# Kernel tuning notes

Measured on AMD Instinct MI355X. Metric: run time of the kernel, lower is better.

The kernel has to match this reference:

```python
import jax, jax.numpy as jnp
import numpy as np

B, S, H = 1, 4096, 2048
NH, NKV, HD = 16, 4, 128  # query heads, kv heads, head_dim
THETA = 1000000.0
NEG = -1e9


def setup_inputs() -> dict:
    key = jax.random.key(0)
    ks = jax.random.split(key, 5)
    hidden_states = jax.random.normal(ks[0], (B, S, H), jnp.float32) * 0.02
    Wq = jax.random.normal(ks[1], (H, NH * HD), jnp.float32) * 0.02
    Wk = jax.random.normal(ks[2], (H, NKV * HD), jnp.float32) * 0.02
    Wv = jax.random.normal(ks[3], (H, NKV * HD), jnp.float32) * 0.02
    Wo = jax.random.normal(ks[4], (H, H), jnp.float32) * 0.02
    # additive causal mask [B,1,S,S]
    causal = jnp.tril(jnp.ones((S, S), bool))
    attention_mask = jnp.where(causal, 0.0, NEG).astype(jnp.float32)[None, None]
    position_ids = jnp.arange(S, dtype=jnp.int32)[None]
    return dict(hidden_states=hidden_states, Wq=Wq, Wk=Wk, Wv=Wv, Wo=Wo,
                attention_mask=attention_mask, position_ids=position_ids)


def _rotate_half(x):
    return jnp.concatenate([-x[..., HD // 2:], x[..., :HD // 2]], axis=-1)


def reference(hidden_states, Wq, Wk, Wv, Wo, attention_mask, position_ids):
    # projections -> [B, heads, S, HD]
    q = (hidden_states @ Wq).reshape(B, S, NH, HD).transpose(0, 2, 1, 3)
    k = (hidden_states @ Wk).reshape(B, S, NKV, HD).transpose(0, 2, 1, 3)
    v = (hidden_states @ Wv).reshape(B, S, NKV, HD).transpose(0, 2, 1, 3)

    # RoPE (HF style: freqs duplicated across halves, rotate_half)
    inv_freq = 1.0 / (THETA ** (jnp.arange(0, HD, 2, dtype=jnp.float32) / HD))
    freqs = position_ids.astype(jnp.float32)[..., None] * inv_freq  # [B,S,HD/2]
    emb = jnp.concatenate([freqs, freqs], axis=-1)                  # [B,S,HD]
    cos = jnp.cos(emb)[:, None].astype(q.dtype)                     # [B,1,S,HD]
    sin = jnp.sin(emb)[:, None].astype(q.dtype)
    q = q * cos + _rotate_half(q) * sin
    k = k * cos + _rotate_half(k) * sin

    # GQA: repeat each kv head consecutively (matches torch repeat_kv)
    rep = NH // NKV
    k = jnp.repeat(k, rep, axis=1)
    v = jnp.repeat(v, rep, axis=1)

    scale = 1.0 / jnp.sqrt(jnp.float32(HD))
    scores = jnp.einsum('bhqd,bhkd->bhqk', q, k) * scale + attention_mask
    attn = jax.nn.softmax(scores.astype(jnp.float32), axis=-1).astype(q.dtype)
    out = jnp.einsum('bhqk,bhkd->bhqd', attn, v)  # [B,NH,S,HD]
    out = out.transpose(0, 2, 1, 3).reshape(B, S, H)
    return out @ Wo
```

## Files before the change

### kernel.cpp

```cpp
#include <hip/hip_runtime.h>
#include <stdint.h>

typedef uint16_t u16;
typedef __bf16  bf16x8 __attribute__((ext_vector_type(8)));
typedef float   f32x4  __attribute__((ext_vector_type(4)));
typedef float   f32x16 __attribute__((ext_vector_type(16)));
typedef uint16_t u16x8 __attribute__((ext_vector_type(8), may_alias));
typedef uint32_t u32x4 __attribute__((ext_vector_type(4)));

typedef const __attribute__((address_space(1))) void* gas_p;
typedef __attribute__((address_space(3))) void* las_p;

#define SCALE2 0.1275430214486847f

__device__ __forceinline__ void load_lds16(const void* g, void* l) {
    __builtin_amdgcn_global_load_lds((gas_p)g, (las_p)l, 16, 0, 0);
}

__device__ __forceinline__ u16 f2bf(float f) {
    uint32_t u = __builtin_bit_cast(uint32_t, f);
    u += 0x7FFFu + ((u >> 16) & 1u);
    return (u16)(u >> 16);
}
__device__ __forceinline__ float bf2f(u16 h) {
    uint32_t u = ((uint32_t)h) << 16;
    return __builtin_bit_cast(float, u);
}
__device__ __forceinline__ bf16x8 ld_frag(const u16* p) {
    u16x8 t = *(const u16x8*)p;
    return __builtin_bit_cast(bf16x8, t);
}
__device__ __forceinline__ uint32_t cvt_pk_bf16(float lo, float hi) {
    uint32_t r;
    asm("v_cvt_pk_bf16_f32 %0, %1, %2" : "=v"(r) : "v"(lo), "v"(hi));
    return r;
}
__device__ __forceinline__ void plane32_swap(uint32_t& a, uint32_t& b) {
    asm("v_permlane32_swap_b32 %0, %1" : "+v"(a), "+v"(b));
}

__global__ __launch_bounds__(256) void convert_hidden(const float* __restrict__ in,
                                                      u16* __restrict__ out, int n8) {
    int i = blockIdx.x * 256 + threadIdx.x;
    if (i >= n8) return;
    const float* p = in + (size_t)i * 8;
    u16x8 o;
#pragma unroll
    for (int j = 0; j < 8; j++) o[j] = f2bf(p[j]);
    *(u16x8*)(out + (size_t)i * 8) = o;
}

__global__ __launch_bounds__(256) void transpose_cvt(const float* __restrict__ in,
                                                     u16* __restrict__ out,
                                                     int R, int C) {
    __shared__ u16 tile[64][65];
    const int tx = threadIdx.x;
    const int bc = blockIdx.x * 64;
    const int br = blockIdx.y * 64;
#pragma unroll
    for (int i = 0; i < 16; i++) {
        int idx = tx + i * 256;
        int r = idx >> 6, c = idx & 63;
        tile[r][c] = f2bf(in[(size_t)(br + r) * C + bc + c]);
    }
    __syncthreads();
#pragma unroll
    for (int i = 0; i < 16; i++) {
        int idx = tx + i * 256;
        int r = idx >> 6, c = idx & 63;
        out[(size_t)(bc + r) * R + br + c] = tile[c][r];
    }
}

__global__ __launch_bounds__(256) void transpose_b16(const u16* __restrict__ in,
                                                     u16* __restrict__ out,
                                                     int R, int C, int ldin, int off) {
    __shared__ u16 tile[64][65];
    const int tx = threadIdx.x;
    const int bc = blockIdx.x * 64;
    const int br = blockIdx.y * 64;
#pragma unroll
    for (int i = 0; i < 16; i++) {
        int idx = tx + i * 256;
        int r = idx >> 6, c = idx & 63;
        tile[r][c] = in[(size_t)(br + r) * ldin + off + bc + c];
    }
    __syncthreads();
#pragma unroll
    for (int i = 0; i < 16; i++) {
        int idx = tx + i * 256;
        int r = idx >> 6, c = idx & 63;
        out[(size_t)(bc + r) * R + br + c] = tile[c][r];
    }
}

#define TM 128
#define TN 128
#define TK 32

__global__ __launch_bounds__(256) void gemm_qkv(const u16* __restrict__ A,
                                                const u16* __restrict__ WqT,
                                                const u16* __restrict__ WkvT,
                                                u16* __restrict__ Qb,
                                                u16* __restrict__ KVb) {
    __shared__ u16 As[TM * TK];
    __shared__ u16 Bs[TN * TK];
    const int K = 2048;
    const int tid  = threadIdx.x;
    const int wave = tid >> 6;
    const int lane = tid & 63;
    const int l15  = lane & 15;
    const int quad = lane >> 4;
    const int m0 = blockIdx.y * TM;
    const int n0 = blockIdx.x * TN;
    const u16* Bt;
    u16* C;
    int ldC, cbase;
    if (n0 < 2048) { Bt = WqT + (size_t)n0 * K;          C = Qb;  ldC = 2048; cbase = n0; }
    else           { Bt = WkvT + (size_t)(n0 - 2048) * K; C = KVb; ldC = 1024; cbase = n0 - 2048; }
    const int wm = (wave >> 1) * 64;
    const int wn = (wave & 1) * 64;

    f32x4 acc[4][4] = {};

    const int srow = tid >> 2;
    const int scol = (tid & 3) * 8;
    const u16* Ap0 = A  + (size_t)(m0 + srow) * K + scol;
    const u16* Ap1 = A  + (size_t)(m0 + 64 + srow) * K + scol;
    const u16* Bp0 = Bt + (size_t)srow * K + scol;
    const u16* Bp1 = Bt + (size_t)(64 + srow) * K + scol;
    u16* AsD0 = As + wave * 512;
    u16* AsD1 = As + 2048 + wave * 512;
    u16* BsD0 = Bs + wave * 512;
    u16* BsD1 = Bs + 2048 + wave * 512;

    for (int k0 = 0; k0 < K; k0 += TK) {
        load_lds16(Ap0 + k0, AsD0);
        load_lds16(Ap1 + k0, AsD1);
        load_lds16(Bp0 + k0, BsD0);
        load_lds16(Bp1 + k0, BsD1);
        __syncthreads();
        bf16x8 af[4], bfr[4];
#pragma unroll
        for (int i = 0; i < 4; i++)
            af[i] = ld_frag(&As[(wm + i * 16 + l15) * TK + quad * 8]);
#pragma unroll
        for (int j = 0; j < 4; j++)
            bfr[j] = ld_frag(&Bs[(wn + j * 16 + l15) * TK + quad * 8]);
#pragma unroll
        for (int i = 0; i < 4; i++)
#pragma unroll
            for (int j = 0; j < 4; j++)
                acc[i][j] = __builtin_amdgcn_mfma_f32_16x16x32_bf16(af[i], bfr[j], acc[i][j], 0, 0, 0);
        __syncthreads();
    }
#pragma unroll
    for (int i = 0; i < 4; i++)
#pragma unroll
        for (int j = 0; j < 4; j++)
#pragma unroll
            for (int r = 0; r < 4; r++) {
                int row = m0 + wm + i * 16 + quad * 4 + r;
                int col = cbase + wn + j * 16 + l15;
                C[(size_t)row * ldC + col] = f2bf(acc[i][j][r]);
            }
}

template <bool F32OUT>
__global__ __launch_bounds__(256) void gemm_bt(const u16* __restrict__ A,
                                               const u16* __restrict__ Bt,
                                               void* __restrict__ Cp,
                                               int M, int N, int K) {
    __shared__ u16 As[TM * TK];
    __shared__ u16 Bs[TN * TK];
    const int tid  = threadIdx.x;
    const int wave = tid >> 6;
    const int lane = tid & 63;
    const int l15  = lane & 15;
    const int quad = lane >> 4;
    const int m0 = blockIdx.y * TM;
    const int n0 = blockIdx.x * TN;
    const int wm = (wave >> 1) * 64;
    const int wn = (wave & 1) * 64;

    f32x4 acc[4][4] = {};

    const int srow = tid >> 2;
    const int scol = (tid & 3) * 8;
    const u16* Ap0 = A  + (size_t)(m0 + srow) * K + scol;
    const u16* Ap1 = A  + (size_t)(m0 + 64 + srow) * K + scol;
    const u16* Bp0 = Bt + (size_t)(n0 + srow) * K + scol;
    const u16* Bp1 = Bt + (size_t)(n0 + 64 + srow) * K + scol;
    u16* AsD0 = As + wave * 512;
    u16* AsD1 = As + 2048 + wave * 512;
    u16* BsD0 = Bs + wave * 512;
    u16* BsD1 = Bs + 2048 + wave * 512;

    for (int k0 = 0; k0 < K; k0 += TK) {
        load_lds16(Ap0 + k0, AsD0);
        load_lds16(Ap1 + k0, AsD1);
        load_lds16(Bp0 + k0, BsD0);
        load_lds16(Bp1 + k0, BsD1);
        __syncthreads();
        bf16x8 af[4], bfr[4];
#pragma unroll
        for (int i = 0; i < 4; i++)
            af[i] = ld_frag(&As[(wm + i * 16 + l15) * TK + quad * 8]);
#pragma unroll
        for (int j = 0; j < 4; j++)
            bfr[j] = ld_frag(&Bs[(wn + j * 16 + l15) * TK + quad * 8]);
#pragma unroll
        for (int i = 0; i < 4; i++)
#pragma unroll
            for (int j = 0; j < 4; j++)
                acc[i][j] = __builtin_amdgcn_mfma_f32_16x16x32_bf16(af[i], bfr[j], acc[i][j], 0, 0, 0);
        __syncthreads();
    }
#pragma unroll
    for (int i = 0; i < 4; i++)
#pragma unroll
        for (int j = 0; j < 4; j++)
#pragma unroll
            for (int r = 0; r < 4; r++) {
                int row = m0 + wm + i * 16 + quad * 4 + r;
                int col = n0 + wn + j * 16 + l15;
                if (F32OUT)
                    ((float*)Cp)[(size_t)row * N + col] = acc[i][j][r];
                else
                    ((u16*)Cp)[(size_t)row * N + col] = f2bf(acc[i][j][r]);
            }
}

__global__ __launch_bounds__(256) void rope_kernel(u16* __restrict__ Q,
                                                   u16* __restrict__ KV) {
    int g = blockIdx.x * 256 + threadIdx.x;
    int d = g & 63;
    int row = g >> 6;
    int s = row / 20;
    int hh = row - s * 20;
    u16* buf = (hh < 16) ? (Q + (size_t)s * 2048 + hh * 128)
                         : (KV + (size_t)s * 1024 + (hh - 16) * 128);
    float p = (float)s;
    float angle = p * exp2f((float)d * (-19.931568569324174f / 64.0f));
    float sc = (hh < 16) ? SCALE2 : 1.0f;
    float c = cosf(angle) * sc, sn = sinf(angle) * sc;
    float x0 = bf2f(buf[d]), x1 = bf2f(buf[d + 64]);
    buf[d]      = f2bf(x0 * c - x1 * sn);
    buf[d + 64] = f2bf(x1 * c + x0 * sn);
}


#define SMAX(CC, SV, QG, PA, LACC, MSK)                                        \
  do {                                                                         \
    float p_[16]; float rs_ = 0.f;                                             \
    const int qrow_ = (QG) + l31;                                              \
    const int kvbs_ = kv0 + (CC) * 32 + 4 * hi8;                               \
    _Pragma("unroll")                                                          \
    for (int r = 0; r < 16; r++) {                                             \
      float pe = exp2f((SV)[r]);                                               \
      if (MSK) { int kvv = kvbs_ + (r & 3) + 8 * (r >> 2);                     \
                 pe = (kvv <= qrow_) ? pe : 0.f; }                             \
      p_[r] = pe; rs_ += pe;                                                   \
    }                                                                          \
    LACC += rs_;                                                               \
    uint32_t w0 = cvt_pk_bf16(p_[0], p_[1]);                                   \
    uint32_t w1 = cvt_pk_bf16(p_[2], p_[3]);                                   \
    uint32_t w2 = cvt_pk_bf16(p_[4], p_[5]);                                   \
    uint32_t w3 = cvt_pk_bf16(p_[6], p_[7]);                                   \
    plane32_swap(w0, w2); plane32_swap(w1, w3);                                \
    uint32_t w4 = cvt_pk_bf16(p_[8], p_[9]);                                   \
    uint32_t w5 = cvt_pk_bf16(p_[10], p_[11]);                                 \
    uint32_t w6 = cvt_pk_bf16(p_[12], p_[13]);                                 \
    uint32_t w7 = cvt_pk_bf16(p_[14], p_[15]);                                 \
    plane32_swap(w4, w6); plane32_swap(w5, w7);                                \
    u32x4 a0_ = {w0, w1, w2, w3}, a1_ = {w4, w5, w6, w7};                      \
    PA[0] = __builtin_bit_cast(bf16x8, a0_);                                   \
    PA[1] = __builtin_bit_cast(bf16x8, a1_);                                   \
  } while (0)

#define QK_CHUNK(CC, DOA, DOB, MSK)                                            \
  do {                                                                         \
    const int krow_ = (CC) * 32 + l31;                                         \
    f32x16 svA_ = {}, svB_ = {};                                               \
    _Pragma("unroll")                                                          \
    for (int dk = 0; dk < 8; dk++) {                                           \
      bf16x8 kf = ld_frag(&Kb[krow_ * 128 + (((dk * 2 + hi8) + krow_) & 15) * 8]); \
      if (DOA) svA_ = __builtin_amdgcn_mfma_f32_32x32x16_bf16(kf, qfA[dk], svA_, 0, 0, 0); \
      if (DOB) svB_ = __builtin_amdgcn_mfma_f32_32x32x16_bf16(kf, qfB[dk], svB_, 0, 0, 0); \
    }                                                                          \
    bf16x8 paA_[2], paB_[2];                                                   \
    if (DOA) SMAX((CC), svA_, qg0A, paA_, lrA, (MSK));                         \
    if (DOB) SMAX((CC), svB_, qg0B, paB_, lrB, (MSK));                         \
    _Pragma("unroll")                                                          \
    for (int ks2 = 0; ks2 < 2; ks2++) {                                        \
      _Pragma("unroll")                                                        \
      for (int nt = 0; nt < 4; nt++) {                                         \
        const int d_ = nt * 32 + l31;                                          \
        bf16x8 vf = ld_frag(&Vb[d_ * 64 + ((((CC) * 4 + ks2 * 2 + hi8) + d_) & 7) * 8]); \
        if (DOA) accA[nt] = __builtin_amdgcn_mfma_f32_32x32x16_bf16(paA_[ks2], vf, accA[nt], 0, 0, 0); \
        if (DOB) accB[nt] = __builtin_amdgcn_mfma_f32_32x32x16_bf16(paB_[ks2], vf, accB[nt], 0, 0, 0); \
      }                                                                        \
    }                                                                          \
  } while (0)

__global__ __launch_bounds__(256, 1) void flash_attn5(const u16* __restrict__ Q,
                                                      const u16* __restrict__ KVb,
                                                      const u16* __restrict__ VT,
                                                      u16* __restrict__ O) {
    __shared__ u16 Ks[2][8192];
    __shared__ u16 Vs[2][8192];
    __shared__ float Llds[4][2][32];
    const int tid  = threadIdx.x;
    const int wave = tid >> 6;
    const int lane = tid & 63;
    const int l31  = lane & 31;
    const int hi8  = lane >> 5;
    const int bx   = blockIdx.x;
    const int h    = blockIdx.y;
    const int kvh  = h >> 2;
    const int qg0A = bx * 128 + wave * 32;
    const int qg0B = 3968 - bx * 128 + wave * 32;
    const int dA   = qg0A >> 6;
    const int dB   = qg0B >> 6;
    const int nkv  = 64 - 2 * bx;

    bf16x8 qfA[8], qfB[8];
    {
        const u16* pa = Q + (size_t)(qg0A + l31) * 2048 + h * 128 + hi8 * 8;
        const u16* pb = Q + (size_t)(qg0B + l31) * 2048 + h * 128 + hi8 * 8;
#pragma unroll
        for (int dk = 0; dk < 8; dk++) {
            qfA[dk] = ld_frag(pa + dk * 16);
            qfB[dk] = ld_frag(pb + dk * 16);
        }
    }

    const u16* srcK[4];
    const u16* srcV[4];
#pragma unroll
    for (int r = 0; r < 4; r++) {
        int p = r * 256 + tid;
        int kv = p >> 4;
        srcK[r] = KVb + (size_t)kv * 1024 + kvh * 128 + ((((p & 15) - kv) & 15) * 8);
        int d = p >> 3;
        srcV[r] = VT + (size_t)(kvh * 128 + d) * 4096 + ((((p & 7) - (d & 7)) & 7) * 8);
    }

    f32x16 accA[4] = {}, accB[4] = {};
    float lrA = 0.f, lrB = 0.f;

#pragma unroll
    for (int r = 0; r < 4; r++) {
        load_lds16(srcK[r], &Ks[0][r * 2048 + wave * 512]);
        load_lds16(srcV[r], &Vs[0][r * 2048 + wave * 512]);
    }
    asm volatile("s_waitcnt vmcnt(0)" ::: "memory");
    __syncthreads();

    for (int kvb = 0; kvb < nkv; kvb++) {
        const int cur = kvb & 1;
        if (kvb + 1 < nkv) {
            const int kvn = (kvb + 1) * 64;
#pragma unroll
            for (int r = 0; r < 4; r++) {
                load_lds16(srcK[r] + (size_t)kvn * 1024, &Ks[cur ^ 1][r * 2048 + wave * 512]);
                load_lds16(srcV[r] + kvn, &Vs[cur ^ 1][r * 2048 + wave * 512]);
            }
        }
        const u16* Kb = Ks[cur];
        const u16* Vb = Vs[cur];
        const int kv0 = kvb * 64;

        if (kvb == dA || kvb == dB) {
            QK_CHUNK(0, 1, 1, 1);
            QK_CHUNK(1, 1, 1, 1);
        } else if (kvb < dA) {
            QK_CHUNK(0, 1, 1, 0);
            QK_CHUNK(1, 1, 1, 0);
        } else if (kvb < dB) {
            QK_CHUNK(0, 0, 1, 0);
            QK_CHUNK(1, 0, 1, 0);
        }

        asm volatile("s_waitcnt vmcnt(0)" ::: "memory");
        __syncthreads();
    }

    float ltA = lrA + __shfl_xor(lrA, 32);
    float ltB = lrB + __shfl_xor(lrB, 32);
    if (lane < 32) {
        Llds[wave][0][l31] = ltA;
        Llds[wave][1][l31] = ltB;
    }
    __syncthreads();
#pragma unroll
    for (int r = 0; r < 16; r++) {
        int qr = (r & 3) + 8 * (r >> 2) + 4 * hi8;
        float liA = 1.0f / Llds[wave][0][qr];
        float liB = 1.0f / Llds[wave][1][qr];
        u16* opA = O + (size_t)(qg0A + qr) * 2048 + h * 128 + l31;
        u16* opB = O + (size_t)(qg0B + qr) * 2048 + h * 128 + l31;
#pragma unroll
        for (int nt = 0; nt < 4; nt++) {
            opA[nt * 32] = f2bf(accA[nt][r] * liA);
            opB[nt * 32] = f2bf(accB[nt][r] * liB);
        }
    }
}

extern "C" void kernel_launch(void* const* d_in, const int* in_sizes, int n_in,
                              void* d_out, int out_size, void* d_ws, size_t ws_size,
                              hipStream_t stream) {
    const float* hidden = (const float*)d_in[0];
    const float* Wq = (const float*)d_in[1];
    const float* Wk = (const float*)d_in[2];
    const float* Wv = (const float*)d_in[3];
    const float* Wo = (const float*)d_in[4];
    float* out = (float*)d_out;

    u16* ws   = (u16*)d_ws;
    u16* Hb   = ws;
    u16* Qb   = Hb   + 8388608;
    u16* KVb  = Qb   + 8388608;
    u16* WqT  = KVb  + 4194304;
    u16* WkvT = WqT  + 4194304;
    u16* VT   = WkvT + 2097152;

    convert_hidden<<<4096, 256, 0, stream>>>(hidden, Hb, 1048576);

    transpose_cvt<<<dim3(32, 32), 256, 0, stream>>>(Wq, WqT, 2048, 2048);
    transpose_cvt<<<dim3(8, 32), 256, 0, stream>>>(Wk, WkvT, 2048, 512);
    transpose_cvt<<<dim3(8, 32), 256, 0, stream>>>(Wv, WkvT + 1048576, 2048, 512);

    gemm_qkv<<<dim3(24, 32), 256, 0, stream>>>(Hb, WqT, WkvT, Qb, KVb);

    u16* WoT = WqT;
    transpose_cvt<<<dim3(32, 32), 256, 0, stream>>>(Wo, WoT, 2048, 2048);

    rope_kernel<<<dim3(20480), 256, 0, stream>>>(Qb, KVb);

    transpose_b16<<<dim3(8, 64), 256, 0, stream>>>(KVb, VT, 4096, 512, 1024, 512);

    u16* Ob = Hb;
    flash_attn5<<<dim3(16, 16), 256, 0, stream>>>(Qb, KVb, VT, Ob);

    gemm_bt<true><<<dim3(16, 32), 256, 0, stream>>>(Ob, WoT, out, 4096, 2048, 2048);
}
```

Measured before the change: 435.0 us.

## Split KV range across two wave groups per block in flash attention

The attention block grows from 4 to 8 waves. Each group of 4 waves handles alternate 64-key blocks of a 128-key pair loaded per iteration, so the same query tiles are processed with twice the wave-level parallelism. This targets low occupancy and latency exposure, since the grid has only 256 blocks. Partial accumulators and row sums from group 1 are reduced through LDS scratch into group 0 before normalization and store. That adds LDS traffic, a larger LDS footprint and an extra barrier at the end. There is also some load imbalance when one group's block lies past the causal diagonal.

```diff
diff --git a/kernel.cpp b/kernel.cpp
--- a/kernel.cpp
+++ b/kernel.cpp
@@ -271,8 +271,9 @@
     uint32_t w4 = cvt_pk_bf16(p_[8], p_[9]);                                   \
     uint32_t w5 = cvt_pk_bf16(p_[10], p_[11]);                                 \
     uint32_t w6 = cvt_pk_bf16(p_[12], p_[13]);                                 \
+    plane32_swap(w4, w6);                                                      \
     uint32_t w7 = cvt_pk_bf16(p_[14], p_[15]);                                 \
-    plane32_swap(w4, w6); plane32_swap(w5, w7);                                \
+    plane32_swap(w5, w7);                                                      \
     u32x4 a0_ = {w0, w1, w2, w3}, a1_ = {w4, w5, w6, w7};                      \
     PA[0] = __builtin_bit_cast(bf16x8, a0_);                                   \
     PA[1] = __builtin_bit_cast(bf16x8, a1_);                                   \
@@ -296,33 +297,36 @@
       _Pragma("unroll")                                                        \
       for (int nt = 0; nt < 4; nt++) {                                         \
         const int d_ = nt * 32 + l31;                                          \
-        bf16x8 vf = ld_frag(&Vb[d_ * 64 + ((((CC) * 4 + ks2 * 2 + hi8) + d_) & 7) * 8]); \
+        const int vc_ = g * 8 + (CC) * 4 + ks2 * 2 + hi8;                      \
+        bf16x8 vf = ld_frag(&Vsp[d_ * 128 + ((vc_ + d_) & 15) * 8]);           \
         if (DOA) accA[nt] = __builtin_amdgcn_mfma_f32_32x32x16_bf16(paA_[ks2], vf, accA[nt], 0, 0, 0); \
         if (DOB) accB[nt] = __builtin_amdgcn_mfma_f32_32x32x16_bf16(paB_[ks2], vf, accB[nt], 0, 0, 0); \
       }                                                                        \
     }                                                                          \
   } while (0)
 
-__global__ __launch_bounds__(256, 1) void flash_attn5(const u16* __restrict__ Q,
+__global__ __launch_bounds__(512, 2) void flash_attn6(const u16* __restrict__ Q,
                                                       const u16* __restrict__ KVb,
                                                       const u16* __restrict__ VT,
                                                       u16* __restrict__ O) {
-    __shared__ u16 Ks[2][8192];
-    __shared__ u16 Vs[2][8192];
-    __shared__ float Llds[4][2][32];
+    __shared__ u16 Ks[2][16384];
+    __shared__ u16 Vs[2][16384];
+    __shared__ float Llds[4][2][2][32];
     const int tid  = threadIdx.x;
-    const int wave = tid >> 6;
+    const int w    = tid >> 6;
+    const int g    = w >> 2;
+    const int ww   = w & 3;
     const int lane = tid & 63;
     const int l31  = lane & 31;
     const int hi8  = lane >> 5;
     const int bx   = blockIdx.x;
     const int h    = blockIdx.y;
     const int kvh  = h >> 2;
-    const int qg0A = bx * 128 + wave * 32;
-    const int qg0B = 3968 - bx * 128 + wave * 32;
+    const int qg0A = bx * 128 + ww * 32;
+    const int qg0B = 3968 - bx * 128 + ww * 32;
     const int dA   = qg0A >> 6;
     const int dB   = qg0B >> 6;
-    const int nkv  = 64 - 2 * bx;
+    const int npairs = 32 - bx;
 
     bf16x8 qfA[8], qfB[8];
     {
@@ -339,11 +343,10 @@
     const u16* srcV[4];
 #pragma unroll
     for (int r = 0; r < 4; r++) {
-        int p = r * 256 + tid;
-        int kv = p >> 4;
-        srcK[r] = KVb + (size_t)kv * 1024 + kvh * 128 + ((((p & 15) - kv) & 15) * 8);
-        int d = p >> 3;
-        srcV[r] = VT + (size_t)(kvh * 128 + d) * 4096 + ((((p & 7) - (d & 7)) & 7) * 8);
+        int p = r * 512 + tid;
+        int rr = p >> 4, c = p & 15;
+        srcK[r] = KVb + (size_t)rr * 1024 + kvh * 128 + (((c - rr) & 15) * 8);
+        srcV[r] = VT + (size_t)(kvh * 128 + rr) * 4096 + (((c - rr) & 15) * 8);
     }
 
     f32x16 accA[4] = {}, accB[4] = {};
@@ -351,35 +354,33 @@
 
 #pragma unroll
     for (int r = 0; r < 4; r++) {
-        load_lds16(srcK[r], &Ks[0][r * 2048 + wave * 512]);
-        load_lds16(srcV[r], &Vs[0][r * 2048 + wave * 512]);
+        load_lds16(srcK[r], &Ks[0][r * 4096 + w * 512]);
+        load_lds16(srcV[r], &Vs[0][r * 4096 + w * 512]);
     }
     asm volatile("s_waitcnt vmcnt(0)" ::: "memory");
     __syncthreads();
 
-    for (int kvb = 0; kvb < nkv; kvb++) {
-        const int cur = kvb & 1;
-        if (kvb + 1 < nkv) {
-            const int kvn = (kvb + 1) * 64;
+    for (int t = 0; t < npairs; t++) {
+        const int cur = t & 1;
+        if (t + 1 < npairs) {
+            const int kvp = (t + 1) * 128;
 #pragma unroll
             for (int r = 0; r < 4; r++) {
-                load_lds16(srcK[r] + (size_t)kvn * 1024, &Ks[cur ^ 1][r * 2048 + wave * 512]);
-                load_lds16(srcV[r] + kvn, &Vs[cur ^ 1][r * 2048 + wave * 512]);
+                load_lds16(srcK[r] + (size_t)kvp * 1024, &Ks[cur ^ 1][r * 4096 + w * 512]);
+                load_lds16(srcV[r] + kvp,                &Vs[cur ^ 1][r * 4096 + w * 512]);
             }
         }
-        const u16* Kb = Ks[cur];
-        const u16* Vb = Vs[cur];
+        const int kvb = 2 * t + g;
+        const u16* Kb  = &Ks[cur][g * 8192];
+        const u16* Vsp = &Vs[cur][0];
         const int kv0 = kvb * 64;
 
-        if (kvb == dA || kvb == dB) {
-            QK_CHUNK(0, 1, 1, 1);
-            QK_CHUNK(1, 1, 1, 1);
-        } else if (kvb < dA) {
-            QK_CHUNK(0, 1, 1, 0);
-            QK_CHUNK(1, 1, 1, 0);
-        } else if (kvb < dB) {
-            QK_CHUNK(0, 0, 1, 0);
-            QK_CHUNK(1, 0, 1, 0);
+        if (kvb <= dA) {
+            if (kvb == dA) { QK_CHUNK(0, 1, 1, 1); QK_CHUNK(1, 1, 1, 1); }
+            else           { QK_CHUNK(0, 1, 1, 0); QK_CHUNK(1, 1, 1, 0); }
+        } else if (kvb <= dB) {
+            if (kvb == dB) { QK_CHUNK(0, 0, 1, 1); QK_CHUNK(1, 0, 1, 1); }
+            else           { QK_CHUNK(0, 0, 1, 0); QK_CHUNK(1, 0, 1, 0); }
         }
 
         asm volatile("s_waitcnt vmcnt(0)" ::: "memory");
@@ -389,21 +390,52 @@
     float ltA = lrA + __shfl_xor(lrA, 32);
     float ltB = lrB + __shfl_xor(lrB, 32);
     if (lane < 32) {
-        Llds[wave][0][l31] = ltA;
-        Llds[wave][1][l31] = ltB;
+        Llds[ww][g][0][l31] = ltA;
+        Llds[ww][g][1][l31] = ltB;
     }
     __syncthreads();
-#pragma unroll
-    for (int r = 0; r < 16; r++) {
-        int qr = (r & 3) + 8 * (r >> 2) + 4 * hi8;
-        float liA = 1.0f / Llds[wave][0][qr];
-        float liB = 1.0f / Llds[wave][1][qr];
-        u16* opA = O + (size_t)(qg0A + qr) * 2048 + h * 128 + l31;
-        u16* opB = O + (size_t)(qg0B + qr) * 2048 + h * 128 + l31;
-#pragma unroll
-        for (int nt = 0; nt < 4; nt++) {
-            opA[nt * 32] = f2bf(accA[nt][r] * liA);
-            opB[nt * 32] = f2bf(accB[nt][r] * liB);
+    float* scrA = (float*)&Ks[0][0];
+    float* scrB = (float*)&Vs[0][0];
+    const int sb = ww * 64 + lane;
+    if (g == 1) {
+#pragma unroll
+        for (int nt = 0; nt < 4; nt++)
+#pragma unroll
+            for (int q = 0; q < 4; q++) {
+                f32x4 a = {accA[nt][q * 4 + 0], accA[nt][q * 4 + 1],
+                           accA[nt][q * 4 + 2], accA[nt][q * 4 + 3]};
+                f32x4 b = {accB[nt][q * 4 + 0], accB[nt][q * 4 + 1],
+                           accB[nt][q * 4 + 2], accB[nt][q * 4 + 3]};
+                *(f32x4*)&scrA[((nt * 4 + q) * 256 + sb) * 4] = a;
+                *(f32x4*)&scrB[((nt * 4 + q) * 256 + sb) * 4] = b;
+            }
+    }
+    __syncthreads();
+    if (g == 0) {
+#pragma unroll
+        for (int nt = 0; nt < 4; nt++)
+#pragma unroll
+            for (int q = 0; q < 4; q++) {
+                f32x4 a = *(const f32x4*)&scrA[((nt * 4 + q) * 256 + sb) * 4];
+                f32x4 b = *(const f32x4*)&scrB[((nt * 4 + q) * 256 + sb) * 4];
+#pragma unroll
+                for (int e = 0; e < 4; e++) {
+                    accA[nt][q * 4 + e] += a[e];
+                    accB[nt][q * 4 + e] += b[e];
+                }
+            }
+#pragma unroll
+        for (int r = 0; r < 16; r++) {
+            int qr = (r & 3) + 8 * (r >> 2) + 4 * hi8;
+            float liA = 1.0f / (Llds[qr & 0 ? 0 : ww][0][0][qr] + Llds[ww][1][0][qr]);
+            float liB = 1.0f / (Llds[ww][0][1][qr] + Llds[ww][1][1][qr]);
+            u16* opA = O + (size_t)(qg0A + qr) * 2048 + h * 128 + l31;
+            u16* opB = O + (size_t)(qg0B + qr) * 2048 + h * 128 + l31;
+#pragma unroll
+            for (int nt = 0; nt < 4; nt++) {
+                opA[nt * 32] = f2bf(accA[nt][r] * liA);
+                opB[nt * 32] = f2bf(accB[nt][r] * liB);
+            }
         }
     }
 }
@@ -442,7 +474,7 @@
     transpose_b16<<<dim3(8, 64), 256, 0, stream>>>(KVb, VT, 4096, 512, 1024, 512);
 
     u16* Ob = Hb;
-    flash_attn5<<<dim3(16, 16), 256, 0, stream>>>(Qb, KVb, VT, Ob);
+    flash_attn6<<<dim3(16, 16), 512, 0, stream>>>(Qb, KVb, VT, Ob);
 
     gemm_bt<true><<<dim3(16, 32), 256, 0, stream>>>(Ob, WoT, out, 4096, 2048, 2048);
 }
```

Result: slower. 633.3 us (+45.6%).

## Split paired causal q-tiles into separate blocks with two blocks per CU

Applied to the files above, without the earlier changes.

The attention kernel previously had each block handle two mirrored 128-row query tiles (a short and a long causal span) so every block did equal work, sharing K/V tile loads between them. The new kernel gives each block a single query tile, launches 512 blocks, and raises launch_bounds to allow 2 blocks per CU. Halving the accumulators and Q fragments per wave frees registers, which is meant to allow more occupancy and latency hiding. In exchange, K/V loads are no longer shared between the two tiles, and block work is now uneven, so the tail depends on how the scheduler orders the blocks.

```diff
diff --git a/kernel.cpp b/kernel.cpp
--- a/kernel.cpp
+++ b/kernel.cpp
@@ -250,19 +250,25 @@
 }
 
 
-#define SMAX(CC, SV, QG, PA, LACC, MSK)                                        \
+#define QK1(CC, MSK)                                                           \
   do {                                                                         \
+    const int krow_ = (CC) * 32 + l31;                                         \
+    f32x16 sv_ = {};                                                           \
+    _Pragma("unroll")                                                          \
+    for (int dk = 0; dk < 8; dk++) {                                           \
+      bf16x8 kf = ld_frag(&Kb[krow_ * 128 + (((dk * 2 + hi8) + krow_) & 15) * 8]); \
+      sv_ = __builtin_amdgcn_mfma_f32_32x32x16_bf16(kf, qf[dk], sv_, 0, 0, 0); \
+    }                                                                          \
     float p_[16]; float rs_ = 0.f;                                             \
-    const int qrow_ = (QG) + l31;                                              \
     const int kvbs_ = kv0 + (CC) * 32 + 4 * hi8;                               \
     _Pragma("unroll")                                                          \
     for (int r = 0; r < 16; r++) {                                             \
-      float pe = exp2f((SV)[r]);                                               \
+      float pe = exp2f(sv_[r]);                                                \
       if (MSK) { int kvv = kvbs_ + (r & 3) + 8 * (r >> 2);                     \
-                 pe = (kvv <= qrow_) ? pe : 0.f; }                             \
+                 pe = (kvv <= qrow) ? pe : 0.f; }                              \
       p_[r] = pe; rs_ += pe;                                                   \
     }                                                                          \
-    LACC += rs_;                                                               \
+    lr += rs_;                                                                 \
     uint32_t w0 = cvt_pk_bf16(p_[0], p_[1]);                                   \
     uint32_t w1 = cvt_pk_bf16(p_[2], p_[3]);                                   \
     uint32_t w2 = cvt_pk_bf16(p_[4], p_[5]);                                   \
@@ -271,68 +277,53 @@
     uint32_t w4 = cvt_pk_bf16(p_[8], p_[9]);                                   \
     uint32_t w5 = cvt_pk_bf16(p_[10], p_[11]);                                 \
     uint32_t w6 = cvt_pk_bf16(p_[12], p_[13]);                                 \
+    plane32_swap(w4, w6);                                                      \
     uint32_t w7 = cvt_pk_bf16(p_[14], p_[15]);                                 \
-    plane32_swap(w4, w6); plane32_swap(w5, w7);                                \
+    plane32_swap(w5, w7);                                                      \
     u32x4 a0_ = {w0, w1, w2, w3}, a1_ = {w4, w5, w6, w7};                      \
-    PA[0] = __builtin_bit_cast(bf16x8, a0_);                                   \
-    PA[1] = __builtin_bit_cast(bf16x8, a1_);                                   \
-  } while (0)
-
-#define QK_CHUNK(CC, DOA, DOB, MSK)                                            \
-  do {                                                                         \
-    const int krow_ = (CC) * 32 + l31;                                         \
-    f32x16 svA_ = {}, svB_ = {};                                               \
-    _Pragma("unroll")                                                          \
-    for (int dk = 0; dk < 8; dk++) {                                           \
-      bf16x8 kf = ld_frag(&Kb[krow_ * 128 + (((dk * 2 + hi8) + krow_) & 15) * 8]); \
-      if (DOA) svA_ = __builtin_amdgcn_mfma_f32_32x32x16_bf16(kf, qfA[dk], svA_, 0, 0, 0); \
-      if (DOB) svB_ = __builtin_amdgcn_mfma_f32_32x32x16_bf16(kf, qfB[dk], svB_, 0, 0, 0); \
-    }                                                                          \
-    bf16x8 paA_[2], paB_[2];                                                   \
-    if (DOA) SMAX((CC), svA_, qg0A, paA_, lrA, (MSK));                         \
-    if (DOB) SMAX((CC), svB_, qg0B, paB_, lrB, (MSK));                         \
+    bf16x8 pa0_ = __builtin_bit_cast(bf16x8, a0_);                             \
+    bf16x8 pa1_ = __builtin_bit_cast(bf16x8, a1_);                             \
     _Pragma("unroll")                                                          \
     for (int ks2 = 0; ks2 < 2; ks2++) {                                        \
+      bf16x8 pa_ = ks2 ? pa1_ : pa0_;                                          \
       _Pragma("unroll")                                                        \
       for (int nt = 0; nt < 4; nt++) {                                         \
         const int d_ = nt * 32 + l31;                                          \
         bf16x8 vf = ld_frag(&Vb[d_ * 64 + ((((CC) * 4 + ks2 * 2 + hi8) + d_) & 7) * 8]); \
-        if (DOA) accA[nt] = __builtin_amdgcn_mfma_f32_32x32x16_bf16(paA_[ks2], vf, accA[nt], 0, 0, 0); \
-        if (DOB) accB[nt] = __builtin_amdgcn_mfma_f32_32x32x16_bf16(paB_[ks2], vf, accB[nt], 0, 0, 0); \
+        acc[nt] = __builtin_amdgcn_mfma_f32_32x32x16_bf16(pa_, vf, acc[nt], 0, 0, 0); \
       }                                                                        \
     }                                                                          \
   } while (0)
 
-__global__ __launch_bounds__(256, 1) void flash_attn5(const u16* __restrict__ Q,
+__global__ __launch_bounds__(256, 2) void flash_attn7(const u16* __restrict__ Q,
                                                       const u16* __restrict__ KVb,
                                                       const u16* __restrict__ VT,
                                                       u16* __restrict__ O) {
     __shared__ u16 Ks[2][8192];
     __shared__ u16 Vs[2][8192];
-    __shared__ float Llds[4][2][32];
+    __shared__ float Llds[4][32];
     const int tid  = threadIdx.x;
-    const int wave = tid >> 6;
+    const int ww   = tid >> 6;
     const int lane = tid & 63;
     const int l31  = lane & 31;
     const int hi8  = lane >> 5;
-    const int bx   = blockIdx.x;
-    const int h    = blockIdx.y;
+    const int bid  = blockIdx.x;
+    const int h    = bid >> 5;
+    const int cls  = bid & 31;
+    const int bx   = cls >> 1;
+    const int z    = cls & 1;
     const int kvh  = h >> 2;
-    const int qg0A = bx * 128 + wave * 32;
-    const int qg0B = 3968 - bx * 128 + wave * 32;
-    const int dA   = qg0A >> 6;
-    const int dB   = qg0B >> 6;
-    const int nkv  = 64 - 2 * bx;
-
-    bf16x8 qfA[8], qfB[8];
+    const int qt0  = z ? (3968 - bx * 128) : (bx * 128);
+    const int qg0  = qt0 + ww * 32;
+    const int qrow = qg0 + l31;
+    const int dW   = qg0 >> 6;
+    const int nkv  = (qt0 >> 6) + 2;
+
+    bf16x8 qf[8];
     {
-        const u16* pa = Q + (size_t)(qg0A + l31) * 2048 + h * 128 + hi8 * 8;
-        const u16* pb = Q + (size_t)(qg0B + l31) * 2048 + h * 128 + hi8 * 8;
-#pragma unroll
-        for (int dk = 0; dk < 8; dk++) {
-            qfA[dk] = ld_frag(pa + dk * 16);
-            qfB[dk] = ld_frag(pb + dk * 16);
-        }
+        const u16* qp = Q + (size_t)qrow * 2048 + h * 128 + hi8 * 8;
+#pragma unroll
+        for (int dk = 0; dk < 8; dk++) qf[dk] = ld_frag(qp + dk * 16);
     }
 
     const u16* srcK[4];
@@ -346,13 +337,13 @@
         srcV[r] = VT + (size_t)(kvh * 128 + d) * 4096 + ((((p & 7) - (d & 7)) & 7) * 8);
     }
 
-    f32x16 accA[4] = {}, accB[4] = {};
-    float lrA = 0.f, lrB = 0.f;
+    f32x16 acc[4] = {};
+    float lr = 0.f;
 
 #pragma unroll
     for (int r = 0; r < 4; r++) {
-        load_lds16(srcK[r], &Ks[0][r * 2048 + wave * 512]);
-        load_lds16(srcV[r], &Vs[0][r * 2048 + wave * 512]);
+        load_lds16(srcK[r], &Ks[0][r * 2048 + ww * 512]);
+        load_lds16(srcV[r], &Vs[0][r * 2048 + ww * 512]);
     }
     asm volatile("s_waitcnt vmcnt(0)" ::: "memory");
     __syncthreads();
@@ -363,48 +354,37 @@
             const int kvn = (kvb + 1) * 64;
 #pragma unroll
             for (int r = 0; r < 4; r++) {
-                load_lds16(srcK[r] + (size_t)kvn * 1024, &Ks[cur ^ 1][r * 2048 + wave * 512]);
-                load_lds16(srcV[r] + kvn, &Vs[cur ^ 1][r * 2048 + wave * 512]);
+                load_lds16(srcK[r] + (size_t)kvn * 1024, &Ks[cur ^ 1][r * 2048 + ww * 512]);
+                load_lds16(srcV[r] + kvn, &Vs[cur ^ 1][r * 2048 + ww * 512]);
             }
         }
         const u16* Kb = Ks[cur];
         const u16* Vb = Vs[cur];
         const int kv0 = kvb * 64;
 
-        if (kvb == dA || kvb == dB) {
-            QK_CHUNK(0, 1, 1, 1);
-            QK_CHUNK(1, 1, 1, 1);
-        } else if (kvb < dA) {
-            QK_CHUNK(0, 1, 1, 0);
-            QK_CHUNK(1, 1, 1, 0);
-        } else if (kvb < dB) {
-            QK_CHUNK(0, 0, 1, 0);
-            QK_CHUNK(1, 0, 1, 0);
+        if (kvb < dW) {
+            QK1(0, 0);
+            QK1(1, 0);
+        } else if (kvb == dW) {
+            QK1(0, 1);
+            QK1(1, 1);
         }
 
         asm volatile("s_waitcnt vmcnt(0)" ::: "memory");
         __syncthreads();
     }
 
-    float ltA = lrA + __shfl_xor(lrA, 32);
-    float ltB = lrB + __shfl_xor(lrB, 32);
-    if (lane < 32) {
-        Llds[wave][0][l31] = ltA;
-        Llds[wave][1][l31] = ltB;
-    }
+    float lt = lr + __shfl_xor(lr, 32);
+    if (lane < 32) Llds[ww][l31] = lt;
     __syncthreads();
 #pragma unroll
     for (int r = 0; r < 16; r++) {
         int qr = (r & 3) + 8 * (r >> 2) + 4 * hi8;
-        float liA = 1.0f / Llds[wave][0][qr];
-        float liB = 1.0f / Llds[wave][1][qr];
-        u16* opA = O + (size_t)(qg0A + qr) * 2048 + h * 128 + l31;
-        u16* opB = O + (size_t)(qg0B + qr) * 2048 + h * 128 + l31;
-#pragma unroll
-        for (int nt = 0; nt < 4; nt++) {
-            opA[nt * 32] = f2bf(accA[nt][r] * liA);
-            opB[nt * 32] = f2bf(accB[nt][r] * liB);
-        }
+        float linv = 1.0f / Llds[ww][qr];
+        u16* op = O + (size_t)(qg0 + qr) * 2048 + h * 128 + l31;
+#pragma unroll
+        for (int nt = 0; nt < 4; nt++)
+            op[nt * 32] = f2bf(acc[nt][r] * linv);
     }
 }
 
@@ -442,7 +422,7 @@
     transpose_b16<<<dim3(8, 64), 256, 0, stream>>>(KVb, VT, 4096, 512, 1024, 512);
 
     u16* Ob = Hb;
-    flash_attn5<<<dim3(16, 16), 256, 0, stream>>>(Qb, KVb, VT, Ob);
+    flash_attn7<<<dim3(512), 256, 0, stream>>>(Qb, KVb, VT, Ob);
 
     gemm_bt<true><<<dim3(16, 32), 256, 0, stream>>>(Ob, WoT, out, 4096, 2048, 2048);
 }
```

Result: no change. 429.5 us (-1.3%).
